# Optimization experiments

Measured on AMD Instinct MI355X. Metric: run time of the kernel, lower is better.

Reference implementation:

```python
import jax, jax.numpy as jnp
import numpy as np

N = 2048
H = 128
W = 128
NEAR = 0.1


def _quat_to_rotmat(q):
    # q: [N,4] (w,x,y,z), normalized -> [N,3,3]
    q = q / jnp.clip(jnp.linalg.norm(q, axis=1, keepdims=True), 1e-8)
    w, x, y, z = q[:, 0], q[:, 1], q[:, 2], q[:, 3]
    xx, yy, zz = x * x, y * y, z * z
    xy, xz, yz = x * y, x * z, y * z
    wx, wy, wz = w * x, w * y, w * z
    r0 = jnp.stack([1 - 2 * (yy + zz), 2 * (xy - wz), 2 * (xz + wy)], axis=1)
    r1 = jnp.stack([2 * (xy + wz), 1 - 2 * (xx + zz), 2 * (yz - wx)], axis=1)
    r2 = jnp.stack([2 * (xz - wy), 2 * (yz + wx), 1 - 2 * (xx + yy)], axis=1)
    return jnp.stack([r0, r1, r2], axis=1)


def _covariance_matrices(log_scales, rotations):
    # R diag(s^2) R^T + 1e-6 I, per Gaussian
    s2 = jnp.exp(2.0 * log_scales)  # scales**2
    R = _quat_to_rotmat(rotations)  # [N,3,3]
    cov = jnp.einsum('nij,nj,nkj->nik', R, s2, R)
    return cov + 1e-6 * jnp.eye(3, dtype=cov.dtype)


def _render(means, cov3d, colors, opacities, intrinsics, camera_to_world, height, width):
    dt = means.dtype
    Rcw = camera_to_world[:3, :3]
    tcw = camera_to_world[:3, 3]
    Rwc = Rcw.T
    twc = -Rwc @ tcw
    p = means @ Rwc.T + twc  # [N,3] camera-space
    x, y, z = p[:, 0], p[:, 1], p[:, 2]
    valid = (z > NEAR).astype(dt)
    zc = jnp.maximum(z, NEAR)
    fx, fy = intrinsics[0, 0], intrinsics[1, 1]
    cx, cy = intrinsics[0, 2], intrinsics[1, 2]
    u = fx * x / zc + cx
    v = fy * y / zc + cy
    # EWA projection Jacobian [N,2,3]
    zeros = jnp.zeros_like(zc)
    J0 = jnp.stack([fx / zc, zeros, -fx * x / (zc * zc)], axis=1)
    J1 = jnp.stack([zeros, fy / zc, -fy * y / (zc * zc)], axis=1)
    J = jnp.stack([J0, J1], axis=1)
    cov_cam = jnp.einsum('ij,njk,lk->nil', Rwc, cov3d, Rwc)  # [N,3,3]
    cov2d = jnp.einsum('nij,njk,nlk->nil', J, cov_cam, J) + 0.3 * jnp.eye(2, dtype=dt)
    a, b, c = cov2d[:, 0, 0], cov2d[:, 0, 1], cov2d[:, 1, 1]
    det = jnp.maximum(a * c - b * b, 1e-12)
    cA, cB, cC = c / det, -b / det, a / det  # conic (inverse 2D covariance)
    # front-to-back depth order; invalid Gaussians pushed to the back
    order = jnp.argsort(jnp.where(valid > 0, zc, jnp.inf))
    u, v = u[order], v[order]
    cA, cB, cC = cA[order], cB[order], cC[order]
    op = (opacities * valid)[order]
    cols = colors[order]
    xs = jnp.arange(width, dtype=dt)
    ys = jnp.arange(height, dtype=dt)
    dx = xs[None, None, :] - u[:, None, None]  # [N,1,W] -> broadcasts
    dy = ys[None, :, None] - v[:, None, None]  # [N,H,1]
    power = (-0.5 * (cA[:, None, None] * dx * dx + cC[:, None, None] * dy * dy)
             - cB[:, None, None] * dx * dy)  # [N,H,W]
    power = jnp.minimum(power, 0.0)
    alpha = jnp.clip(op[:, None, None] * jnp.exp(power), 0.0, 0.99)
    Tcum = jnp.cumprod(1.0 - alpha, axis=0)
    Texcl = jnp.concatenate([jnp.ones_like(Tcum[:1]), Tcum[:-1]], axis=0)
    weight = alpha * Texcl  # [N,H,W]
    img = jnp.einsum('nhw,nc->hwc', weight, cols)  # [H,W,3]
    return img


def setup_inputs():
    key = jax.random.key(0)
    k = jax.random.split(key, 6)
    xy = jax.random.uniform(k[0], (N, 2), minval=-2.0, maxval=2.0)
    z = jax.random.uniform(k[1], (N, 1), minval=3.0, maxval=9.0)
    means = jnp.concatenate([xy, z], axis=1)
    log_scales = jnp.log(jax.random.uniform(k[2], (N, 3), minval=0.02, maxval=0.2))
    rotations = jax.random.normal(k[3], (N, 4))
    colors = jax.random.uniform(k[4], (N, 3))
    opacities = jax.random.normal(k[5], (N,))
    intrinsics = jnp.array([[150.0, 0.0, W / 2], [0.0, 150.0, H / 2], [0.0, 0.0, 1.0]], dtype=jnp.float32)
    camera_to_world = jnp.eye(4, dtype=jnp.float32)
    return {"means": means, "log_scales": log_scales, "rotations": rotations,
            "colors": colors, "opacities": opacities, "intrinsics": intrinsics,
            "camera_to_world": camera_to_world, "height": H, "width": W}


def reference(means, log_scales, rotations, colors, opacities, intrinsics, camera_to_world, height, width):
    cov3d = _covariance_matrices(log_scales, rotations)
    return _render(means, cov3d, jnp.clip(colors, 0.0, 1.0), jax.nn.sigmoid(opacities),
                   intrinsics, camera_to_world, height, width)
```

## Files before the change

kernel.cpp:

```cpp
#include <hip/hip_runtime.h>
#include <hip/hip_bf16.h>

#define NMAX 2048
#define HH 128
#define WW 128
#define NSEG 8
#define SEG 256
#define NEARP 0.1f

static __device__ __forceinline__ float ldin(const void* p, int i, bool is32) {
    return is32 ? ((const float*)p)[i]
                : __bfloat162float(((const __hip_bfloat16*)p)[i]);
}
static __device__ __forceinline__ bool detect32(const void* intr) {
    return ((const float*)intr)[0] > 1.0f;
}
static __device__ __forceinline__ void stout(void* out, int i, float v, bool is32) {
    if (is32) ((float*)out)[i] = v;
    else      ((__hip_bfloat16*)out)[i] = __float2bfloat16(v);
}


__global__ __launch_bounds__(256) void gs_preprocess(
    const void* __restrict__ means,
    const void* __restrict__ log_scales,
    const void* __restrict__ rots,
    const void* __restrict__ colors,
    const void* __restrict__ opac,
    const void* __restrict__ intr,
    const void* __restrict__ c2w,
    int n,
    unsigned long long* __restrict__ keys,
    float* __restrict__ params)
{
    int i = blockIdx.x * blockDim.x + threadIdx.x;
    if (i >= NMAX) return;
    bool is32 = detect32(intr);
    if (i >= n) {
        keys[i] = (((unsigned long long)0x7f800000u) << 32) | (unsigned int)i;
        return;
    }

    float Rwc[3][3], twc[3];
    {
        float Rcw[3][3], tcw[3];
        for (int r = 0; r < 3; ++r) {
            for (int c = 0; c < 3; ++c) Rcw[r][c] = ldin(c2w, r * 4 + c, is32);
            tcw[r] = ldin(c2w, r * 4 + 3, is32);
        }
        for (int r = 0; r < 3; ++r)
            for (int c = 0; c < 3; ++c) Rwc[r][c] = Rcw[c][r];
        for (int r = 0; r < 3; ++r)
            twc[r] = -(Rwc[r][0] * tcw[0] + Rwc[r][1] * tcw[1] + Rwc[r][2] * tcw[2]);
    }
    float fx = ldin(intr, 0, is32), fy = ldin(intr, 4, is32);
    float cx = ldin(intr, 2, is32), cy = ldin(intr, 5, is32);

    float mx = ldin(means, 3 * i, is32), my = ldin(means, 3 * i + 1, is32),
          mz = ldin(means, 3 * i + 2, is32);
    float px = Rwc[0][0] * mx + Rwc[0][1] * my + Rwc[0][2] * mz + twc[0];
    float py = Rwc[1][0] * mx + Rwc[1][1] * my + Rwc[1][2] * mz + twc[1];
    float pz = Rwc[2][0] * mx + Rwc[2][1] * my + Rwc[2][2] * mz + twc[2];
    bool valid = pz > NEARP;
    float zc = fmaxf(pz, NEARP);
    float izc = 1.0f / zc;
    float u = fx * px * izc + cx;
    float v = fy * py * izc + cy;

    float qw = ldin(rots, 4 * i, is32), qx = ldin(rots, 4 * i + 1, is32),
          qy = ldin(rots, 4 * i + 2, is32), qz = ldin(rots, 4 * i + 3, is32);
    float nrm = sqrtf(qw * qw + qx * qx + qy * qy + qz * qz);
    float inv = 1.0f / fmaxf(nrm, 1e-8f);
    qw *= inv; qx *= inv; qy *= inv; qz *= inv;
    float xx = qx * qx, yy = qy * qy, zz = qz * qz;
    float xy = qx * qy, xz = qx * qz, yz = qy * qz;
    float wx = qw * qx, wy = qw * qy, wz = qw * qz;
    float R[3][3] = {
        {1.f - 2.f * (yy + zz), 2.f * (xy - wz),       2.f * (xz + wy)},
        {2.f * (xy + wz),       1.f - 2.f * (xx + zz), 2.f * (yz - wx)},
        {2.f * (xz - wy),       2.f * (yz + wx),       1.f - 2.f * (xx + yy)}
    };
    float s2[3];
    for (int k = 0; k < 3; ++k) s2[k] = __expf(2.0f * ldin(log_scales, 3 * i + k, is32));

    float M[3][3];
    for (int r = 0; r < 3; ++r)
        for (int c = 0; c < 3; ++c)
            M[r][c] = R[r][0] * s2[0] * R[c][0] + R[r][1] * s2[1] * R[c][1]
                    + R[r][2] * s2[2] * R[c][2];
    M[0][0] += 1e-6f; M[1][1] += 1e-6f; M[2][2] += 1e-6f;

    float TM[3][3];
    for (int r = 0; r < 3; ++r)
        for (int c = 0; c < 3; ++c)
            TM[r][c] = Rwc[r][0] * M[0][c] + Rwc[r][1] * M[1][c] + Rwc[r][2] * M[2][c];
    float CC[3][3];
    for (int r = 0; r < 3; ++r)
        for (int c = 0; c < 3; ++c)
            CC[r][c] = TM[r][0] * Rwc[c][0] + TM[r][1] * Rwc[c][1] + TM[r][2] * Rwc[c][2];

    float J0[3] = {fx * izc, 0.0f, -fx * px * izc * izc};
    float J1[3] = {0.0f, fy * izc, -fy * py * izc * izc};
    float t0[3], t1[3];
    for (int c = 0; c < 3; ++c) {
        t0[c] = J0[0] * CC[0][c] + J0[1] * CC[1][c] + J0[2] * CC[2][c];
        t1[c] = J1[0] * CC[0][c] + J1[1] * CC[1][c] + J1[2] * CC[2][c];
    }
    float a  = t0[0] * J0[0] + t0[1] * J0[1] + t0[2] * J0[2] + 0.3f;
    float bq = t0[0] * J1[0] + t0[1] * J1[1] + t0[2] * J1[2];
    float cq = t1[0] * J1[0] + t1[1] * J1[1] + t1[2] * J1[2] + 0.3f;
    float det = fmaxf(a * cq - bq * bq, 1e-12f);
    float idet = 1.0f / det;
    float cA = cq * idet, cB = -bq * idet, cCc = a * idet;

    float o  = ldin(opac, i, is32);
    float op = valid ? (1.0f / (1.0f + __expf(-o))) : 0.0f;
    float cr = fminf(fmaxf(ldin(colors, 3 * i, is32), 0.f), 1.f);
    float cg = fminf(fmaxf(ldin(colors, 3 * i + 1, is32), 0.f), 1.f);
    float cb = fminf(fmaxf(ldin(colors, 3 * i + 2, is32), 0.f), 1.f);

    float zkey = valid ? zc : __builtin_inff();
    keys[i] = (((unsigned long long)__float_as_uint(zkey)) << 32) | (unsigned int)i;

    float* p = params + i * 12;
    p[0] = u;  p[1] = v;
    p[2] = -0.5f * cA;
    p[3] = -cB;
    p[4] = -0.5f * cCc;
    p[5] = op;
    p[6] = cr; p[7] = cg; p[8] = cb; p[9] = 0.f; p[10] = 0.f; p[11] = 0.f;
}

__global__ __launch_bounds__(256) void gs_rank_scatter(
    const unsigned long long* __restrict__ keys_in,
    const float* __restrict__ params_in,
    float* __restrict__ params_sorted,
    int n)
{
    __shared__ unsigned long long sk[NMAX];
    __shared__ int pr[32][9];
    __shared__ int rk[32];
    int t = threadIdx.x;
    #pragma unroll
    for (int e = 0; e < 8; ++e) sk[t + e * 256] = keys_in[t + e * 256];
    __syncthreads();

    int g0 = blockIdx.x * 32;
    int gi = t >> 3;
    int c  = t & 7;
    unsigned long long mykey = sk[g0 + gi];
    int cnt = 0;
    #pragma unroll 8
    for (int j = c; j < NMAX; j += 8)
        cnt += (sk[j] < mykey) ? 1 : 0;
    pr[gi][c] = cnt;
    __syncthreads();

    if (t < 32) {
        int r = 0;
        #pragma unroll
        for (int k = 0; k < 8; ++k) r += pr[t][k];
        rk[t] = r;
    }
    __syncthreads();

    if (t < 96) {
        int g = t / 3, q = t % 3;
        int src = g0 + g;
        float4 val;
        if (src < n) val = ((const float4*)params_in)[src * 3 + q];
        else         val = make_float4(0.f, 0.f, 0.f, 0.f);
        ((float4*)params_sorted)[rk[g] * 3 + q] = val;
    }
}

__global__ __launch_bounds__(256) void gs_render(
    const float* __restrict__ params_sorted,
    float4* __restrict__ segbuf)
{
    __shared__ float sp[SEG * 12];
    int seg = blockIdx.y;
    int t = threadIdx.x;

    const float4* src = (const float4*)(params_sorted + seg * SEG * 12);
    float4* dst = (float4*)sp;
    #pragma unroll
    for (int k = t; k < SEG * 3; k += 256) dst[k] = src[k];
    __syncthreads();

    int pid0 = (blockIdx.x * 256 + t) * 2;
    float px0 = (float)(pid0 & (WW - 1));
    float px1 = px0 + 1.0f;
    float py  = (float)(pid0 >> 7);

    float T0 = 1.f, r0 = 0.f, g0 = 0.f, b0 = 0.f;
    float T1 = 1.f, r1 = 0.f, g1 = 0.f, b1 = 0.f;
    #pragma unroll 4
    for (int i = 0; i < SEG; ++i) {
        const float* gp = sp + i * 12;
        float4 A = *(const float4*)(gp);
        float4 B = *(const float4*)(gp + 4);
        float4 C = *(const float4*)(gp + 8);
        float dy    = py - A.y;
        float nbdy  = A.w * dy;
        float ncdy2 = (B.x * dy) * dy;

        float dx0 = px0 - A.x;
        float p0 = fmaf(fmaf(A.z, dx0, nbdy), dx0, ncdy2);
        p0 = fminf(p0, 0.0f);
        float al0 = fminf(B.y * __expf(p0), 0.99f);
        float w0 = al0 * T0;
        r0 = fmaf(w0, B.z, r0);
        g0 = fmaf(w0, B.w, g0);
        b0 = fmaf(w0, C.x, b0);
        T0 *= (1.0f - al0);

        float dx1 = px1 - A.x;
        float p1 = fmaf(fmaf(A.z, dx1, nbdy), dx1, ncdy2);
        p1 = fminf(p1, 0.0f);
        float al1 = fminf(B.y * __expf(p1), 0.99f);
        float w1 = al1 * T1;
        r1 = fmaf(w1, B.z, r1);
        g1 = fmaf(w1, B.w, g1);
        b1 = fmaf(w1, C.x, b1);
        T1 *= (1.0f - al1);
    }
    segbuf[seg * (HH * WW) + pid0]     = make_float4(r0, g0, b0, T0);
    segbuf[seg * (HH * WW) + pid0 + 1] = make_float4(r1, g1, b1, T1);
}

__global__ __launch_bounds__(256) void gs_combine(
    const float4* __restrict__ segbuf,
    void* __restrict__ out,
    const void* __restrict__ intr)
{
    int pid = blockIdx.x * 256 + threadIdx.x;
    if (pid >= HH * WW) return;
    bool is32 = detect32(intr);
    float r = 0.f, g = 0.f, b = 0.f, T = 1.0f;
    #pragma unroll
    for (int s = 0; s < NSEG; ++s) {
        float4 vv = segbuf[s * (HH * WW) + pid];
        r = fmaf(T, vv.x, r);
        g = fmaf(T, vv.y, g);
        b = fmaf(T, vv.z, b);
        T *= vv.w;
    }
    stout(out, pid * 3 + 0, r, is32);
    stout(out, pid * 3 + 1, g, is32);
    stout(out, pid * 3 + 2, b, is32);
}

__global__ __launch_bounds__(256) void gs_render_all(
    const float* __restrict__ params_sorted,
    void* __restrict__ out,
    const void* __restrict__ intr)
{
    __shared__ float sp[SEG * 12];
    int t = threadIdx.x;
    int pid = blockIdx.x * 256 + t;
    bool is32 = detect32(intr);
    float pxf = (float)(pid & (WW - 1));
    float pyf = (float)(pid >> 7);

    float T = 1.f, r = 0.f, g = 0.f, b = 0.f;
    for (int seg = 0; seg < NSEG; ++seg) {
        __syncthreads();
        const float4* src = (const float4*)(params_sorted + seg * SEG * 12);
        float4* dst = (float4*)sp;
        #pragma unroll
        for (int k = t; k < SEG * 3; k += 256) dst[k] = src[k];
        __syncthreads();
        for (int i = 0; i < SEG; ++i) {
            const float* gp = sp + i * 12;
            float dx = pxf - gp[0];
            float dy = pyf - gp[1];
            float pwr = fmaf(fmaf(gp[2], dx, gp[3] * dy), dx, (gp[4] * dy) * dy);
            pwr = fminf(pwr, 0.0f);
            float alpha = fminf(gp[5] * __expf(pwr), 0.99f);
            float wgt = alpha * T;
            r = fmaf(wgt, gp[6], r);
            g = fmaf(wgt, gp[7], g);
            b = fmaf(wgt, gp[8], b);
            T *= (1.0f - alpha);
        }
    }
    stout(out, pid * 3 + 0, r, is32);
    stout(out, pid * 3 + 1, g, is32);
    stout(out, pid * 3 + 2, b, is32);
}

extern "C" void kernel_launch(void* const* d_in, const int* in_sizes, int n_in,
                              void* d_out, int out_size, void* d_ws, size_t ws_size,
                              hipStream_t stream)
{
    const void* means      = d_in[0];
    const void* log_scales = d_in[1];
    const void* rotations  = d_in[2];
    const void* colors     = d_in[3];
    const void* opacities  = d_in[4];
    const void* intrinsics = d_in[5];
    const void* cam2world  = d_in[6];

    int n = in_sizes[4];
    if (n > NMAX) n = NMAX;

    size_t off_keys   = 0;
    size_t off_params = NMAX * 8;
    size_t off_sorted = off_params + NMAX * 48;
    size_t off_seg    = off_sorted + NMAX * 48;
    size_t need_seg   = off_seg + (size_t)NSEG * HH * WW * 16;

    unsigned long long* keys = (unsigned long long*)((char*)d_ws + off_keys);
    float* params  = (float*)((char*)d_ws + off_params);
    float* sortedp = (float*)((char*)d_ws + off_sorted);
    float4* segbuf = (float4*)((char*)d_ws + off_seg);

    gs_preprocess<<<NMAX / 256, 256, 0, stream>>>(
        means, log_scales, rotations, colors, opacities, intrinsics, cam2world,
        n, keys, params);
    gs_rank_scatter<<<NMAX / 32, 256, 0, stream>>>(keys, params, sortedp, n);

    if (ws_size >= need_seg) {
        dim3 rg(HH * WW / 512, NSEG);
        gs_render<<<rg, 256, 0, stream>>>(sortedp, segbuf);
        gs_combine<<<HH * WW / 256, 256, 0, stream>>>(segbuf, d_out, intrinsics);
    } else {
        gs_render_all<<<HH * WW / 256, 256, 0, stream>>>(sortedp, d_out, intrinsics);
    }
}
```

Measured before the change: 99.00 us.

## Fuse preprocess into rank kernel and fuse segmented render with combine

Folds the per-Gaussian preprocessing into the rank/scatter kernel: every block recomputes depth keys for all Gaussians, and the first 32 threads fully preprocess that block's 32 Gaussians into shared memory before scattering them to sorted order. The render and combine kernels merge into a single kernel in which each block handles 64 pixels with 4 thread groups, each group compositing a quarter of the depth-sorted Gaussians. The partial results are combined in shared memory, which removes the global segment buffer round trip and two kernel launches. The costs are redundant depth-key computation in every block and 4x fewer pixels per block, so only 256 blocks are launched and each thread processes 512 Gaussians serially.

```diff
diff --git a/kernel.cpp b/kernel.cpp
--- a/kernel.cpp
+++ b/kernel.cpp
@@ -4,8 +4,6 @@
 #define NMAX 2048
 #define HH 128
 #define WW 128
-#define NSEG 8
-#define SEG 256
 #define NEARP 0.1f
 
 static __device__ __forceinline__ float ldin(const void* p, int i, bool is32) {
@@ -21,26 +19,11 @@
 }
 
 
-__global__ __launch_bounds__(256) void gs_preprocess(
-    const void* __restrict__ means,
-    const void* __restrict__ log_scales,
-    const void* __restrict__ rots,
-    const void* __restrict__ colors,
-    const void* __restrict__ opac,
-    const void* __restrict__ intr,
-    const void* __restrict__ c2w,
-    int n,
-    unsigned long long* __restrict__ keys,
-    float* __restrict__ params)
-{
-    int i = blockIdx.x * blockDim.x + threadIdx.x;
-    if (i >= NMAX) return;
-    bool is32 = detect32(intr);
-    if (i >= n) {
-        keys[i] = (((unsigned long long)0x7f800000u) << 32) | (unsigned int)i;
-        return;
-    }
-
+static __device__ void preprocess_one(
+    const void* means, const void* log_scales, const void* rots,
+    const void* colors, const void* opac, const void* intr, const void* c2w,
+    int i, bool is32, float* rec)
+{
     float Rwc[3][3], twc[3];
     {
         float Rcw[3][3], tcw[3];
@@ -115,45 +98,86 @@
 
     float o  = ldin(opac, i, is32);
     float op = valid ? (1.0f / (1.0f + __expf(-o))) : 0.0f;
-    float cr = fminf(fmaxf(ldin(colors, 3 * i, is32), 0.f), 1.f);
-    float cg = fminf(fmaxf(ldin(colors, 3 * i + 1, is32), 0.f), 1.f);
-    float cb = fminf(fmaxf(ldin(colors, 3 * i + 2, is32), 0.f), 1.f);
-
-    float zkey = valid ? zc : __builtin_inff();
-    keys[i] = (((unsigned long long)__float_as_uint(zkey)) << 32) | (unsigned int)i;
-
-    float* p = params + i * 12;
-    p[0] = u;  p[1] = v;
-    p[2] = -0.5f * cA;
-    p[3] = -cB;
-    p[4] = -0.5f * cCc;
-    p[5] = op;
-    p[6] = cr; p[7] = cg; p[8] = cb; p[9] = 0.f; p[10] = 0.f; p[11] = 0.f;
-}
-
-__global__ __launch_bounds__(256) void gs_rank_scatter(
-    const unsigned long long* __restrict__ keys_in,
-    const float* __restrict__ params_in,
-    float* __restrict__ params_sorted,
-    int n)
+    rec[0] = u;  rec[1] = v;
+    rec[2] = -0.5f * cA;
+    rec[3] = -cB;
+    rec[4] = -0.5f * cCc;
+    rec[5] = op;
+    rec[6] = fminf(fmaxf(ldin(colors, 3 * i, is32), 0.f), 1.f);
+    rec[7] = fminf(fmaxf(ldin(colors, 3 * i + 1, is32), 0.f), 1.f);
+    rec[8] = fminf(fmaxf(ldin(colors, 3 * i + 2, is32), 0.f), 1.f);
+    rec[9] = 0.f; rec[10] = 0.f; rec[11] = 0.f;
+}
+
+__global__ __launch_bounds__(256) void gs_prep_rank(
+    const void* __restrict__ means,
+    const void* __restrict__ log_scales,
+    const void* __restrict__ rots,
+    const void* __restrict__ colors,
+    const void* __restrict__ opac,
+    const void* __restrict__ intr,
+    const void* __restrict__ c2w,
+    int n,
+    float* __restrict__ params_sorted)
 {
     __shared__ unsigned long long sk[NMAX];
+    __shared__ float sp32[32][12];
     __shared__ int pr[32][9];
     __shared__ int rk[32];
     int t = threadIdx.x;
-    #pragma unroll
-    for (int e = 0; e < 8; ++e) sk[t + e * 256] = keys_in[t + e * 256];
+    bool is32 = detect32(intr);
+
+    {
+        float r20 = ldin(c2w, 2, is32);
+        float r21 = ldin(c2w, 6, is32);
+        float r22 = ldin(c2w, 10, is32);
+        float tc0 = ldin(c2w, 3, is32), tc1 = ldin(c2w, 7, is32), tc2 = ldin(c2w, 11, is32);
+        float tw2 = -(r20 * tc0 + r21 * tc1 + r22 * tc2);
+        #pragma unroll
+        for (int e = 0; e < 8; ++e) {
+            int i = t + e * 256;
+            unsigned long long key;
+            if (i < n) {
+                float mx = ldin(means, 3 * i, is32);
+                float my = ldin(means, 3 * i + 1, is32);
+                float mz = ldin(means, 3 * i + 2, is32);
+                float pz = r20 * mx + r21 * my + r22 * mz + tw2;
+                float zc = fmaxf(pz, NEARP);
+                float zkey = (pz > NEARP) ? zc : __builtin_inff();
+                key = (((unsigned long long)__float_as_uint(zkey)) << 32) | (unsigned int)i;
+            } else {
+                key = (((unsigned long long)0x7f800000u) << 32) | (unsigned int)i;
+            }
+            sk[i] = key;
+        }
+    }
     __syncthreads();
 
     int g0 = blockIdx.x * 32;
-    int gi = t >> 3;
-    int c  = t & 7;
-    unsigned long long mykey = sk[g0 + gi];
-    int cnt = 0;
-    #pragma unroll 8
-    for (int j = c; j < NMAX; j += 8)
-        cnt += (sk[j] < mykey) ? 1 : 0;
-    pr[gi][c] = cnt;
+
+    if (t < 32) {
+        int i = g0 + t;
+        float rec[12];
+        if (i < n) {
+            preprocess_one(means, log_scales, rots, colors, opac, intr, c2w, i, is32, rec);
+        } else {
+            #pragma unroll
+            for (int k = 0; k < 12; ++k) rec[k] = 0.f;
+        }
+        #pragma unroll
+        for (int k = 0; k < 12; ++k) sp32[t][k] = rec[k];
+    }
+
+    {
+        int gi = t >> 3;
+        int c  = t & 7;
+        unsigned long long mykey = sk[g0 + gi];
+        int cnt = 0;
+        #pragma unroll 8
+        for (int j = c; j < NMAX; j += 8)
+            cnt += (sk[j] < mykey) ? 1 : 0;
+        pr[gi][c] = cnt;
+    }
     __syncthreads();
 
     if (t < 32) {
@@ -166,128 +190,77 @@
 
     if (t < 96) {
         int g = t / 3, q = t % 3;
-        int src = g0 + g;
-        float4 val;
-        if (src < n) val = ((const float4*)params_in)[src * 3 + q];
-        else         val = make_float4(0.f, 0.f, 0.f, 0.f);
-        ((float4*)params_sorted)[rk[g] * 3 + q] = val;
-    }
-}
-
-__global__ __launch_bounds__(256) void gs_render(
-    const float* __restrict__ params_sorted,
-    float4* __restrict__ segbuf)
-{
-    __shared__ float sp[SEG * 12];
-    int seg = blockIdx.y;
-    int t = threadIdx.x;
-
-    const float4* src = (const float4*)(params_sorted + seg * SEG * 12);
-    float4* dst = (float4*)sp;
-    #pragma unroll
-    for (int k = t; k < SEG * 3; k += 256) dst[k] = src[k];
-    __syncthreads();
-
-    int pid0 = (blockIdx.x * 256 + t) * 2;
-    float px0 = (float)(pid0 & (WW - 1));
-    float px1 = px0 + 1.0f;
-    float py  = (float)(pid0 >> 7);
-
-    float T0 = 1.f, r0 = 0.f, g0 = 0.f, b0 = 0.f;
-    float T1 = 1.f, r1 = 0.f, g1 = 0.f, b1 = 0.f;
-    #pragma unroll 4
-    for (int i = 0; i < SEG; ++i) {
-        const float* gp = sp + i * 12;
-        float4 A = *(const float4*)(gp);
-        float4 B = *(const float4*)(gp + 4);
-        float4 C = *(const float4*)(gp + 8);
-        float dy    = py - A.y;
-        float nbdy  = A.w * dy;
-        float ncdy2 = (B.x * dy) * dy;
-
-        float dx0 = px0 - A.x;
-        float p0 = fmaf(fmaf(A.z, dx0, nbdy), dx0, ncdy2);
-        p0 = fminf(p0, 0.0f);
-        float al0 = fminf(B.y * __expf(p0), 0.99f);
-        float w0 = al0 * T0;
-        r0 = fmaf(w0, B.z, r0);
-        g0 = fmaf(w0, B.w, g0);
-        b0 = fmaf(w0, C.x, b0);
-        T0 *= (1.0f - al0);
-
-        float dx1 = px1 - A.x;
-        float p1 = fmaf(fmaf(A.z, dx1, nbdy), dx1, ncdy2);
-        p1 = fminf(p1, 0.0f);
-        float al1 = fminf(B.y * __expf(p1), 0.99f);
-        float w1 = al1 * T1;
-        r1 = fmaf(w1, B.z, r1);
-        g1 = fmaf(w1, B.w, g1);
-        b1 = fmaf(w1, C.x, b1);
-        T1 *= (1.0f - al1);
-    }
-    segbuf[seg * (HH * WW) + pid0]     = make_float4(r0, g0, b0, T0);
-    segbuf[seg * (HH * WW) + pid0 + 1] = make_float4(r1, g1, b1, T1);
-}
-
-__global__ __launch_bounds__(256) void gs_combine(
-    const float4* __restrict__ segbuf,
-    void* __restrict__ out,
-    const void* __restrict__ intr)
-{
-    int pid = blockIdx.x * 256 + threadIdx.x;
-    if (pid >= HH * WW) return;
-    bool is32 = detect32(intr);
-    float r = 0.f, g = 0.f, b = 0.f, T = 1.0f;
-    #pragma unroll
-    for (int s = 0; s < NSEG; ++s) {
-        float4 vv = segbuf[s * (HH * WW) + pid];
-        r = fmaf(T, vv.x, r);
-        g = fmaf(T, vv.y, g);
-        b = fmaf(T, vv.z, b);
-        T *= vv.w;
-    }
-    stout(out, pid * 3 + 0, r, is32);
-    stout(out, pid * 3 + 1, g, is32);
-    stout(out, pid * 3 + 2, b, is32);
-}
-
-__global__ __launch_bounds__(256) void gs_render_all(
+        ((float4*)params_sorted)[rk[g] * 3 + q] = ((const float4*)sp32[g])[q];
+    }
+}
+
+__global__ __launch_bounds__(256) void gs_render_fused(
     const float* __restrict__ params_sorted,
     void* __restrict__ out,
     const void* __restrict__ intr)
 {
-    __shared__ float sp[SEG * 12];
+    __shared__ float sp[512 * 12];
+    __shared__ float4 res[4][64];
     int t = threadIdx.x;
-    int pid = blockIdx.x * 256 + t;
-    bool is32 = detect32(intr);
+    int q = t >> 6;
+    int p = t & 63;
+    int pid = blockIdx.x * 64 + p;
     float pxf = (float)(pid & (WW - 1));
     float pyf = (float)(pid >> 7);
 
     float T = 1.f, r = 0.f, g = 0.f, b = 0.f;
-    for (int seg = 0; seg < NSEG; ++seg) {
+    for (int k = 0; k < 4; ++k) {
         __syncthreads();
-        const float4* src = (const float4*)(params_sorted + seg * SEG * 12);
-        float4* dst = (float4*)sp;
-        #pragma unroll
-        for (int k = t; k < SEG * 3; k += 256) dst[k] = src[k];
+        #pragma unroll
+        for (int j = t; j < 1536; j += 256) {
+            int qq = j / 384;
+            int w  = j - qq * 384;
+            ((float4*)sp)[qq * 384 + w] =
+                ((const float4*)params_sorted)[(qq * 512 + k * 128) * 3 + w];
+        }
         __syncthreads();
-        for (int i = 0; i < SEG; ++i) {
-            const float* gp = sp + i * 12;
-            float dx = pxf - gp[0];
-            float dy = pyf - gp[1];
-            float pwr = fmaf(fmaf(gp[2], dx, gp[3] * dy), dx, (gp[4] * dy) * dy);
-            pwr = fminf(pwr, 0.0f);
-            float alpha = fminf(gp[5] * __expf(pwr), 0.99f);
-            float wgt = alpha * T;
-            r = fmaf(wgt, gp[6], r);
-            g = fmaf(wgt, gp[7], g);
-            b = fmaf(wgt, gp[8], b);
-            T *= (1.0f - alpha);
-        }
-    }
-    stout(out, pid * 3 + 0, r, is32);
-    stout(out, pid * 3 + 1, g, is32);
-    stout(out, pid * 3 + 2, b, is32);
+
+        const float* base = sp + q * 128 * 12;
+        #pragma unroll 4
+        for (int i = 0; i < 128; ++i) {
+            const float* gp = base + i * 12;
+            float4 A = *(const float4*)(gp);
+            float4 B = *(const float4*)(gp + 4);
+            float4 C = *(const float4*)(gp + 8);
+            float dy    = pyf - A.y;
+            float nbdy  = A.w * dy;
+            float ncdy2 = (B.x * dy) * dy;
+            float dx = pxf - A.x;
+            float pw = fmaf(fmaf(A.z, dx, nbdy), dx, ncdy2);
+            pw = fminf(pw, 0.0f);
+            float al = fminf(B.y * __expf(pw), 0.99f);
+            float w0 = al * T;
+            r = fmaf(w0, B.z, r);
+            g = fmaf(w0, B.w, g);
+            b = fmaf(w0, C.x, b);
+            T *= (1.0f - al);
+        }
+    }
+    res[q][p] = make_float4(r, g, b, T);
+    __syncthreads();
+
+    if (t < 64) {
+        bool is32 = detect32(intr);
+        float4 a0 = res[0][t];
+        float rr = a0.x, gg = a0.y, bb = a0.z, Tt = a0.w;
+        #pragma unroll
+        for (int s = 1; s < 4; ++s) {
+            float4 as = res[s][t];
+            rr = fmaf(Tt, as.x, rr);
+            gg = fmaf(Tt, as.y, gg);
+            bb = fmaf(Tt, as.z, bb);
+            Tt *= as.w;
+        }
+        int opid = blockIdx.x * 64 + t;
+        stout(out, opid * 3 + 0, rr, is32);
+        stout(out, opid * 3 + 1, gg, is32);
+        stout(out, opid * 3 + 2, bb, is32);
+    }
 }
 
 extern "C" void kernel_launch(void* const* d_in, const int* in_sizes, int n_in,
@@ -304,28 +277,12 @@
 
     int n = in_sizes[4];
     if (n > NMAX) n = NMAX;
-
-    size_t off_keys   = 0;
-    size_t off_params = NMAX * 8;
-    size_t off_sorted = off_params + NMAX * 48;
-    size_t off_seg    = off_sorted + NMAX * 48;
-    size_t need_seg   = off_seg + (size_t)NSEG * HH * WW * 16;
-
-    unsigned long long* keys = (unsigned long long*)((char*)d_ws + off_keys);
-    float* params  = (float*)((char*)d_ws + off_params);
-    float* sortedp = (float*)((char*)d_ws + off_sorted);
-    float4* segbuf = (float4*)((char*)d_ws + off_seg);
-
-    gs_preprocess<<<NMAX / 256, 256, 0, stream>>>(
+    if (ws_size < (size_t)NMAX * 48) return;
+
+    float* sortedp = (float*)d_ws;
+
+    gs_prep_rank<<<NMAX / 32, 256, 0, stream>>>(
         means, log_scales, rotations, colors, opacities, intrinsics, cam2world,
-        n, keys, params);
-    gs_rank_scatter<<<NMAX / 32, 256, 0, stream>>>(keys, params, sortedp, n);
-
-    if (ws_size >= need_seg) {
-        dim3 rg(HH * WW / 512, NSEG);
-        gs_render<<<rg, 256, 0, stream>>>(sortedp, segbuf);
-        gs_combine<<<HH * WW / 256, 256, 0, stream>>>(segbuf, d_out, intrinsics);
-    } else {
-        gs_render_all<<<HH * WW / 256, 256, 0, stream>>>(sortedp, d_out, intrinsics);
-    }
-}
+        n, sortedp);
+    gs_render_fused<<<HH * WW / 64, 256, 0, stream>>>(sortedp, d_out, intrinsics);
+}
```

After: 108.0 us. +9.1%, slower.

## Fuse preprocess into rank-scatter kernel, recomputing depth keys per block

Applied to the files above, without the earlier changes.

Merges the preprocessing and rank/scatter kernels into one launch. Each block recomputes camera-space depth keys for all Gaussians directly from the means, and one warp computes the full parameters for the block's 32 Gaussians into shared memory before scattering them to sorted positions. This removes a kernel launch and the global round-trip for keys and unsorted params. In exchange, each block redundantly reads all means and computes keys, and warp 0 serially does both the preprocessing and its share of the rank counting.

```diff
diff --git a/kernel.cpp b/kernel.cpp
--- a/kernel.cpp
+++ b/kernel.cpp
@@ -21,26 +21,11 @@
 }
 
 
-__global__ __launch_bounds__(256) void gs_preprocess(
-    const void* __restrict__ means,
-    const void* __restrict__ log_scales,
-    const void* __restrict__ rots,
-    const void* __restrict__ colors,
-    const void* __restrict__ opac,
-    const void* __restrict__ intr,
-    const void* __restrict__ c2w,
-    int n,
-    unsigned long long* __restrict__ keys,
-    float* __restrict__ params)
-{
-    int i = blockIdx.x * blockDim.x + threadIdx.x;
-    if (i >= NMAX) return;
-    bool is32 = detect32(intr);
-    if (i >= n) {
-        keys[i] = (((unsigned long long)0x7f800000u) << 32) | (unsigned int)i;
-        return;
-    }
-
+static __device__ void preprocess_one(
+    const void* means, const void* log_scales, const void* rots,
+    const void* colors, const void* opac, const void* intr, const void* c2w,
+    int i, bool is32, float* rec)
+{
     float Rwc[3][3], twc[3];
     {
         float Rcw[3][3], tcw[3];
@@ -115,45 +100,86 @@
 
     float o  = ldin(opac, i, is32);
     float op = valid ? (1.0f / (1.0f + __expf(-o))) : 0.0f;
-    float cr = fminf(fmaxf(ldin(colors, 3 * i, is32), 0.f), 1.f);
-    float cg = fminf(fmaxf(ldin(colors, 3 * i + 1, is32), 0.f), 1.f);
-    float cb = fminf(fmaxf(ldin(colors, 3 * i + 2, is32), 0.f), 1.f);
-
-    float zkey = valid ? zc : __builtin_inff();
-    keys[i] = (((unsigned long long)__float_as_uint(zkey)) << 32) | (unsigned int)i;
-
-    float* p = params + i * 12;
-    p[0] = u;  p[1] = v;
-    p[2] = -0.5f * cA;
-    p[3] = -cB;
-    p[4] = -0.5f * cCc;
-    p[5] = op;
-    p[6] = cr; p[7] = cg; p[8] = cb; p[9] = 0.f; p[10] = 0.f; p[11] = 0.f;
-}
-
-__global__ __launch_bounds__(256) void gs_rank_scatter(
-    const unsigned long long* __restrict__ keys_in,
-    const float* __restrict__ params_in,
-    float* __restrict__ params_sorted,
-    int n)
+    rec[0] = u;  rec[1] = v;
+    rec[2] = -0.5f * cA;
+    rec[3] = -cB;
+    rec[4] = -0.5f * cCc;
+    rec[5] = op;
+    rec[6] = fminf(fmaxf(ldin(colors, 3 * i, is32), 0.f), 1.f);
+    rec[7] = fminf(fmaxf(ldin(colors, 3 * i + 1, is32), 0.f), 1.f);
+    rec[8] = fminf(fmaxf(ldin(colors, 3 * i + 2, is32), 0.f), 1.f);
+    rec[9] = 0.f; rec[10] = 0.f; rec[11] = 0.f;
+}
+
+__global__ __launch_bounds__(256) void gs_prep_rank(
+    const void* __restrict__ means,
+    const void* __restrict__ log_scales,
+    const void* __restrict__ rots,
+    const void* __restrict__ colors,
+    const void* __restrict__ opac,
+    const void* __restrict__ intr,
+    const void* __restrict__ c2w,
+    int n,
+    float* __restrict__ params_sorted)
 {
     __shared__ unsigned long long sk[NMAX];
+    __shared__ float sp32[32][12];
     __shared__ int pr[32][9];
     __shared__ int rk[32];
     int t = threadIdx.x;
-    #pragma unroll
-    for (int e = 0; e < 8; ++e) sk[t + e * 256] = keys_in[t + e * 256];
+    bool is32 = detect32(intr);
+
+    {
+        float r20 = ldin(c2w, 2, is32);
+        float r21 = ldin(c2w, 6, is32);
+        float r22 = ldin(c2w, 10, is32);
+        float tc0 = ldin(c2w, 3, is32), tc1 = ldin(c2w, 7, is32), tc2 = ldin(c2w, 11, is32);
+        float tw2 = -(r20 * tc0 + r21 * tc1 + r22 * tc2);
+        #pragma unroll
+        for (int e = 0; e < 8; ++e) {
+            int i = t + e * 256;
+            unsigned long long key;
+            if (i < n) {
+                float mx = ldin(means, 3 * i, is32);
+                float my = ldin(means, 3 * i + 1, is32);
+                float mz = ldin(means, 3 * i + 2, is32);
+                float pz = r20 * mx + r21 * my + r22 * mz + tw2;
+                float zc = fmaxf(pz, NEARP);
+                float zkey = (pz > NEARP) ? zc : __builtin_inff();
+                key = (((unsigned long long)__float_as_uint(zkey)) << 32) | (unsigned int)i;
+            } else {
+                key = (((unsigned long long)0x7f800000u) << 32) | (unsigned int)i;
+            }
+            sk[i] = key;
+        }
+    }
     __syncthreads();
 
     int g0 = blockIdx.x * 32;
-    int gi = t >> 3;
-    int c  = t & 7;
-    unsigned long long mykey = sk[g0 + gi];
-    int cnt = 0;
-    #pragma unroll 8
-    for (int j = c; j < NMAX; j += 8)
-        cnt += (sk[j] < mykey) ? 1 : 0;
-    pr[gi][c] = cnt;
+
+    if (t < 32) {
+        int i = g0 + t;
+        float rec[12];
+        if (i < n) {
+            preprocess_one(means, log_scales, rots, colors, opac, intr, c2w, i, is32, rec);
+        } else {
+            #pragma unroll
+            for (int k = 0; k < 12; ++k) rec[k] = 0.f;
+        }
+        #pragma unroll
+        for (int k = 0; k < 12; ++k) sp32[t][k] = rec[k];
+    }
+
+    {
+        int gi = t >> 3;
+        int c  = t & 7;
+        unsigned long long mykey = sk[g0 + gi];
+        int cnt = 0;
+        #pragma unroll 8
+        for (int j = c; j < NMAX; j += 8)
+            cnt += (sk[j] < mykey) ? 1 : 0;
+        pr[gi][c] = cnt;
+    }
     __syncthreads();
 
     if (t < 32) {
@@ -166,11 +192,7 @@
 
     if (t < 96) {
         int g = t / 3, q = t % 3;
-        int src = g0 + g;
-        float4 val;
-        if (src < n) val = ((const float4*)params_in)[src * 3 + q];
-        else         val = make_float4(0.f, 0.f, 0.f, 0.f);
-        ((float4*)params_sorted)[rk[g] * 3 + q] = val;
+        ((float4*)params_sorted)[rk[g] * 3 + q] = ((const float4*)sp32[g])[q];
     }
 }
 
@@ -305,21 +327,16 @@
     int n = in_sizes[4];
     if (n > NMAX) n = NMAX;
 
-    size_t off_keys   = 0;
-    size_t off_params = NMAX * 8;
-    size_t off_sorted = off_params + NMAX * 48;
-    size_t off_seg    = off_sorted + NMAX * 48;
+    size_t off_sorted = 0;
+    size_t off_seg    = (size_t)NMAX * 48;
     size_t need_seg   = off_seg + (size_t)NSEG * HH * WW * 16;
 
-    unsigned long long* keys = (unsigned long long*)((char*)d_ws + off_keys);
-    float* params  = (float*)((char*)d_ws + off_params);
     float* sortedp = (float*)((char*)d_ws + off_sorted);
     float4* segbuf = (float4*)((char*)d_ws + off_seg);
 
-    gs_preprocess<<<NMAX / 256, 256, 0, stream>>>(
+    gs_prep_rank<<<NMAX / 32, 256, 0, stream>>>(
         means, log_scales, rotations, colors, opacities, intrinsics, cam2world,
-        n, keys, params);
-    gs_rank_scatter<<<NMAX / 32, 256, 0, stream>>>(keys, params, sortedp, n);
+        n, sortedp);
 
     if (ws_size >= need_seg) {
         dim3 rg(HH * WW / 512, NSEG);
```

New measurement: 100.4 us. Within noise of the previous version (+1.4%).
